# Performance work log

Hardware: AMD Instinct MI355X
Metric: run time of the kernel (lower is better)

The kernel has to match this reference:

```python
import jax, jax.numpy as jnp
import numpy as np

B, D, H = 32768, 256, 256
LEAKY = 0.2  # tf.nn.leaky_relu default alpha


def setup_inputs() -> dict:
    key = jax.random.key(0)
    ks = jax.random.split(key, 12)
    s = 0.05  # weight scale (original inits comm net to zeros; random keeps grads nonzero)
    return {
        "x": jax.random.normal(ks[0], (B, D), jnp.float32),
        "visible_states_indices": jax.random.randint(ks[1], (B, 1), 0, B, jnp.int32),
        "real_step": jnp.ones((1,), jnp.bool_),
        "h": jax.random.normal(ks[2], (B, H), jnp.float32),
        "c": jax.random.normal(ks[3], (B, H), jnp.float32),
        "W1": s * jax.random.normal(ks[4], (2 * H, 512), jnp.float32),
        "b1": jnp.zeros((512,), jnp.float32),
        "W2": s * jax.random.normal(ks[5], (512, 512), jnp.float32),
        "b2": jnp.zeros((512,), jnp.float32),
        "W3": s * jax.random.normal(ks[6], (512, H), jnp.float32),
        "b3": jnp.zeros((H,), jnp.float32),
        "Wk": s * jax.random.normal(ks[7], (D, 4 * H), jnp.float32),
        "Wr": s * jax.random.normal(ks[8], (H, 4 * H), jnp.float32),
        "bl": jnp.zeros((4 * H,), jnp.float32),
    }


def reference(x, visible_states_indices, real_step, h, c,
              W1, b1, W2, b2, W3, b3, Wk, Wr, bl):
    vid = jnp.squeeze(visible_states_indices, axis=1)          # [B]
    rs = jnp.reshape(real_step, ())                            # scalar bool

    # gather neighbor comm states with a pad row for idx == -1
    padded = jnp.pad(h, ((1, 0), (0, 0)))                      # [B+1, H]
    gathered = jnp.take(padded, vid + 1, axis=0)               # [B, H]

    cs = jnp.concatenate([h, gathered], axis=-1)               # [B, 2H]
    for W, b in ((W1, b1), (W2, b2), (W3, b3)):
        cs = jax.nn.leaky_relu(cs @ W + b, negative_slope=LEAKY)

    # conditional scatter-combine back into the h state
    final_h = jnp.where((vid >= 0)[:, None], h + cs, h)        # [B, H]

    # wrapped LSTM cell (keras LSTMCell gate ordering i, f, g, o)
    z = x @ Wk + final_h @ Wr + bl                             # [B, 4H]
    i, f, g, o = jnp.split(z, 4, axis=-1)
    c_new = jax.nn.sigmoid(f) * c + jax.nn.sigmoid(i) * jnp.tanh(g)
    h_new = jax.nn.sigmoid(o) * jnp.tanh(c_new)
    outputs = h_new

    # only commit new states on real steps
    h_out = jnp.where(rs, h_new, final_h)
    c_out = jnp.where(rs, c_new, c)
    return outputs, h_out, c_out
```

## Files before the change

### kernel.cpp

```cpp
#include <hip/hip_runtime.h>
#include <stdint.h>

#define LEAKY 0.2f
#define NB 32768
#define HD 256

typedef __attribute__((ext_vector_type(8))) short short8;
typedef __attribute__((ext_vector_type(8))) unsigned short ushort8;
typedef __attribute__((ext_vector_type(4))) float f4;

static __device__ __forceinline__ float bf2f(unsigned short u) {
  union { unsigned int i; float f; } v; v.i = ((unsigned int)u) << 16; return v.f;
}
static __device__ __forceinline__ unsigned short f2bf(float f) {
  union { float f; unsigned int i; } v; v.f = f;
  return (unsigned short)((v.i + 0x7fffu + ((v.i >> 16) & 1u)) >> 16);
}
static __device__ __forceinline__ ushort8 pack8(f4 a, f4 b) {
  ushort8 o;
  o[0] = f2bf(a[0]); o[1] = f2bf(a[1]); o[2] = f2bf(a[2]); o[3] = f2bf(a[3]);
  o[4] = f2bf(b[0]); o[5] = f2bf(b[1]); o[6] = f2bf(b[2]); o[7] = f2bf(b[3]);
  return o;
}
static __device__ __forceinline__ float sigm(float x) { return 1.f / (1.f + __expf(-x)); }
static __device__ __forceinline__ float tanha(float x) {
  float e = __expf(2.f * x);
  return 1.f - 2.f / (e + 1.f);
}

__device__ __forceinline__ void gload16(const void* g, void* s) {
  __builtin_amdgcn_global_load_lds(
      (const __attribute__((address_space(1))) unsigned int*)g,
      (__attribute__((address_space(3))) unsigned int*)s, 16, 0, 0);
}

__global__ void wprep(const float* __restrict__ W1, const float* __restrict__ W2,
                      const float* __restrict__ W3, const float* __restrict__ Wk,
                      const float* __restrict__ Wr,
                      unsigned short* __restrict__ W1t, unsigned short* __restrict__ W2t,
                      unsigned short* __restrict__ W3t, unsigned short* __restrict__ Wkrt) {
  int idx = blockIdx.x * 256 + threadIdx.x;
  if (idx < 262144) {
    int n = idx >> 9, k = idx & 511;
    W1t[idx] = f2bf(W1[k * 512 + n]);
  } else if (idx < 524288) {
    int j = idx - 262144;
    int n = j >> 9, k = j & 511;
    W2t[j] = f2bf(W2[k * 512 + n]);
  } else if (idx < 655360) {
    int j = idx - 524288;
    int n = j >> 9, k = j & 511;
    W3t[j] = f2bf(W3[k * 256 + n]);
  } else {
    int j = idx - 655360;
    int rbt = j >> 9, k = j & 511;
    int gate = (rbt >> 4) & 3;
    int hcol = (rbt >> 7) * 32 + ((rbt >> 6) & 1) * 16 + (rbt & 15);
    int ocol = gate * 256 + hcol;
    float v = (k < 256) ? Wk[k * 1024 + ocol] : Wr[(k - 256) * 1024 + ocol];
    Wkrt[j] = f2bf(v);
  }
}

__global__ void build_rows(const float* __restrict__ x, const float* __restrict__ h,
                           const int* __restrict__ vid,
                           unsigned short* __restrict__ catb,
                           unsigned short* __restrict__ csb) {
  int idx = blockIdx.x * 256 + threadIdx.x;
  int m = idx >> 5;
  int j = (idx & 31) << 3;
  f4 a0 = *(const f4*)(x + (size_t)m * 256 + j);
  f4 a1 = *(const f4*)(x + (size_t)m * 256 + j + 4);
  *(ushort8*)(catb + (size_t)m * 512 + j) = pack8(a0, a1);
  f4 h0 = *(const f4*)(h + (size_t)m * 256 + j);
  f4 h1 = *(const f4*)(h + (size_t)m * 256 + j + 4);
  *(ushort8*)(csb + (size_t)m * 512 + j) = pack8(h0, h1);
  int id = vid[m];
  f4 g0 = {0.f, 0.f, 0.f, 0.f}, g1 = {0.f, 0.f, 0.f, 0.f};
  if (id >= 0) {
    g0 = *(const f4*)(h + (size_t)id * 256 + j);
    g1 = *(const f4*)(h + (size_t)id * 256 + j + 4);
  }
  *(ushort8*)(csb + (size_t)m * 512 + 256 + j) = pack8(g0, g1);
}

template <int MODE>
__global__ __launch_bounds__(256, 2) void gemm_bf16(
    const unsigned short* __restrict__ A,
    const unsigned short* __restrict__ Bt,
    const float* __restrict__ bias,
    int nTn, int K,
    unsigned short* __restrict__ outb, int ldo, int col_off,
    float* __restrict__ outf,
    const float* __restrict__ hst,
    const int* __restrict__ vid,
    const float* __restrict__ cin,
    const unsigned char* __restrict__ rsp) {
  __shared__ unsigned short sA[128 * 64];
  __shared__ unsigned short sB[128 * 64];

  const int t = threadIdx.x;
  const int tm = blockIdx.x / nTn;
  const int tn = blockIdx.x - tm * nTn;
  const int wid = t >> 6, lane = t & 63;
  const int wr = wid >> 1, wc = wid & 1;
  const int lrow = lane & 15, lkhi = lane >> 4;

  const unsigned short* Asrc = A + (size_t)tm * 128 * K;
  const unsigned short* Bsrc = Bt + (size_t)tn * 128 * K;
  const int rsub = t >> 3, slot = t & 7;

  f4 acc[4][4];
#pragma unroll
  for (int i = 0; i < 4; ++i)
#pragma unroll
    for (int j = 0; j < 4; ++j) acc[i][j] = {0.f, 0.f, 0.f, 0.f};

  for (int k0 = 0; k0 < K; k0 += 64) {
#pragma unroll
    for (int iss = 0; iss < 4; ++iss) {
      int r = iss * 32 + rsub;
      int gs = slot ^ (r & 7);
      gload16(Asrc + (size_t)r * K + k0 + gs * 8, (char*)sA + r * 128 + slot * 16);
      gload16(Bsrc + (size_t)r * K + k0 + gs * 8, (char*)sB + r * 128 + slot * 16);
    }
    __syncthreads();
#pragma unroll
    for (int kk = 0; kk < 2; ++kk) {
      short8 af[4], bfr[4];
#pragma unroll
      for (int mi = 0; mi < 4; ++mi) {
        int row = wr * 64 + mi * 16 + lrow;
        int s = (kk * 4 + lkhi) ^ (row & 7);
        af[mi] = *(const short8*)&sA[row * 64 + s * 8];
      }
#pragma unroll
      for (int ni = 0; ni < 4; ++ni) {
        int rn = wc * 64 + ni * 16 + lrow;
        int s = (kk * 4 + lkhi) ^ (rn & 7);
        bfr[ni] = *(const short8*)&sB[rn * 64 + s * 8];
      }
#pragma unroll
      for (int mi = 0; mi < 4; ++mi)
#pragma unroll
        for (int ni = 0; ni < 4; ++ni)
          acc[mi][ni] = __builtin_amdgcn_mfma_f32_16x16x32_bf16(af[mi], bfr[ni],
                                                                acc[mi][ni], 0, 0, 0);
    }
    __syncthreads();
  }

  const int m_base = tm * 128 + wr * 64;
  const int n_base = tn * 128 + wc * 64;
  if (MODE == 1) {
#pragma unroll
    for (int mi = 0; mi < 4; ++mi) {
#pragma unroll
      for (int r = 0; r < 4; ++r) {
        int row = m_base + mi * 16 + lkhi * 4 + r;
        int id = vid[row];
#pragma unroll
        for (int ni = 0; ni < 4; ++ni) {
          int col = n_base + ni * 16 + lrow;
          float v = acc[mi][ni][r] + bias[col];
          v = v > 0.f ? v : LEAKY * v;
          float hv = hst[(size_t)row * HD + col];
          float fh = (id >= 0) ? hv + v : hv;
          outf[(size_t)row * HD + col] = fh;
          outb[(size_t)row * ldo + col_off + col] = f2bf(fh);
        }
      }
    }
  } else if (MODE == 3) {
    const bool real = rsp[0] != 0;
    const int hcol = tn * 32 + wc * 16 + lrow;
    const float bi = bias[hcol];
    const float bff = bias[256 + hcol];
    const float bg = bias[512 + hcol];
    const float bo = bias[768 + hcol];
    float* outs = outf;
    float* houtp = outf + (size_t)NB * HD;
    float* coutp = outf + (size_t)2 * NB * HD;
#pragma unroll
    for (int mi = 0; mi < 4; ++mi) {
#pragma unroll
      for (int r = 0; r < 4; ++r) {
        int row = m_base + mi * 16 + lkhi * 4 + r;
        size_t base = (size_t)row * HD + hcol;
        float cold = cin[base];
        float i_ = sigm(acc[mi][0][r] + bi);
        float f_ = sigm(acc[mi][1][r] + bff);
        float g_ = tanha(acc[mi][2][r] + bg);
        float o_ = sigm(acc[mi][3][r] + bo);
        float cv = f_ * cold + i_ * g_;
        float hv = o_ * tanha(cv);
        outs[base] = hv;
        if (real) {
          houtp[base] = hv;
          coutp[base] = cv;
        } else {
          coutp[base] = cold;
        }
      }
    }
  } else {
#pragma unroll
    for (int ni = 0; ni < 4; ++ni) {
      int col = n_base + ni * 16 + lrow;
      float bia = bias[col];
#pragma unroll
      for (int mi = 0; mi < 4; ++mi) {
#pragma unroll
        for (int r = 0; r < 4; ++r) {
          int row = m_base + mi * 16 + lkhi * 4 + r;
          float v = acc[mi][ni][r] + bia;
          v = v > 0.f ? v : LEAKY * v;
          outb[(size_t)row * ldo + col_off + col] = f2bf(v);
        }
      }
    }
  }
}

extern "C" void kernel_launch(void* const* d_in, const int* in_sizes, int n_in,
                              void* d_out, int out_size, void* d_ws, size_t ws_size,
                              hipStream_t stream) {
  const float* x = (const float*)d_in[0];
  const int* vid = (const int*)d_in[1];
  const unsigned char* rs = (const unsigned char*)d_in[2];
  const float* h = (const float*)d_in[3];
  const float* c = (const float*)d_in[4];
  const float* W1 = (const float*)d_in[5];
  const float* b1 = (const float*)d_in[6];
  const float* W2 = (const float*)d_in[7];
  const float* b2 = (const float*)d_in[8];
  const float* W3 = (const float*)d_in[9];
  const float* b3 = (const float*)d_in[10];
  const float* Wk = (const float*)d_in[11];
  const float* Wr = (const float*)d_in[12];
  const float* bl = (const float*)d_in[13];
  float* dout = (float*)d_out;

  char* ws = (char*)d_ws;
  unsigned short* W1t = (unsigned short*)(ws);
  unsigned short* W2t = (unsigned short*)(ws + 524288);
  unsigned short* W3t = (unsigned short*)(ws + 1048576);
  unsigned short* Wkrt = (unsigned short*)(ws + 1310720);
  unsigned short* bufA = (unsigned short*)(ws + 2359296);
  unsigned short* bufB = (unsigned short*)(ws + 2359296 + 33554432);
  unsigned short* catb = (unsigned short*)(ws + 2359296 + 67108864);

  float* fhout = dout + (size_t)NB * HD;

  wprep<<<4608, 256, 0, stream>>>(W1, W2, W3, Wk, Wr, W1t, W2t, W3t, Wkrt);
  build_rows<<<NB * 32 / 256, 256, 0, stream>>>(x, h, vid, catb, bufA);

  gemm_bf16<0><<<(NB / 128) * 4, 256, 0, stream>>>(
      bufA, W1t, b1, 4, 512, bufB, 512, 0, nullptr, nullptr, nullptr, nullptr, nullptr);
  gemm_bf16<0><<<(NB / 128) * 4, 256, 0, stream>>>(
      bufB, W2t, b2, 4, 512, bufA, 512, 0, nullptr, nullptr, nullptr, nullptr, nullptr);
  gemm_bf16<1><<<(NB / 128) * 2, 256, 0, stream>>>(
      bufA, W3t, b3, 2, 512, catb, 512, 256, fhout, h, vid, nullptr, nullptr);
  gemm_bf16<3><<<(NB / 128) * 8, 256, 0, stream>>>(
      catb, Wkrt, bl, 8, 512, nullptr, 0, 0, dout, nullptr, nullptr, c, rs);
}
```

Baseline: 351.3 us.

## Tile weight transpose through LDS, remap GEMM blocks per XCD, raise occupancy

The weight-prep kernel now transposes 64x64 tiles through shared memory, so reads and bf16 writes are coalesced instead of strided. The GEMM block index is remapped so that all N-tiles of one M row-tile land on the same XCD, which should improve L2 reuse of the A tile. NTN becomes a template parameter and launch bounds rise from 2 to 4 blocks per CU. The higher occupancy target may cause register spills in the 4x4 accumulator GEMM.

After: 345.2 us. No clear change (-1.7%).

```diff
diff --git a/kernel.cpp b/kernel.cpp
--- a/kernel.cpp
+++ b/kernel.cpp
@@ -39,26 +39,52 @@
                       const float* __restrict__ Wr,
                       unsigned short* __restrict__ W1t, unsigned short* __restrict__ W2t,
                       unsigned short* __restrict__ W3t, unsigned short* __restrict__ Wkrt) {
-  int idx = blockIdx.x * 256 + threadIdx.x;
-  if (idx < 262144) {
-    int n = idx >> 9, k = idx & 511;
-    W1t[idx] = f2bf(W1[k * 512 + n]);
-  } else if (idx < 524288) {
-    int j = idx - 262144;
-    int n = j >> 9, k = j & 511;
-    W2t[j] = f2bf(W2[k * 512 + n]);
-  } else if (idx < 655360) {
-    int j = idx - 524288;
-    int n = j >> 9, k = j & 511;
-    W3t[j] = f2bf(W3[k * 256 + n]);
+  __shared__ float tile[64][65];
+  const int id = blockIdx.x, t = threadIdx.x;
+  const int tr = t >> 6, tc = t & 63;
+
+  const float* src;
+  unsigned short* dst;
+  int kbase, nbase, srcld, perm = 0;
+  if (id < 64) {
+    src = W1; dst = W1t; srcld = 512;
+    kbase = (id >> 3) * 64; nbase = (id & 7) * 64;
+  } else if (id < 128) {
+    src = W2; dst = W2t; srcld = 512;
+    kbase = ((id - 64) >> 3) * 64; nbase = ((id - 64) & 7) * 64;
+  } else if (id < 160) {
+    src = W3; dst = W3t; srcld = 256;
+    kbase = ((id - 128) >> 2) * 64; nbase = ((id - 128) & 3) * 64;
   } else {
-    int j = idx - 655360;
-    int rbt = j >> 9, k = j & 511;
-    int gate = (rbt >> 4) & 3;
-    int hcol = (rbt >> 7) * 32 + ((rbt >> 6) & 1) * 16 + (rbt & 15);
-    int ocol = gate * 256 + hcol;
-    float v = (k < 256) ? Wk[k * 1024 + ocol] : Wr[(k - 256) * 1024 + ocol];
-    Wkrt[j] = f2bf(v);
+    src = nullptr; dst = Wkrt; srcld = 1024; perm = 1;
+    kbase = ((id - 160) >> 4) * 64; nbase = ((id - 160) & 15) * 64;
+  }
+
+#pragma unroll
+  for (int p = 0; p < 16; ++p) {
+    int r = p * 4 + tr;
+    int k = kbase + r, n = nbase + tc;
+    float v;
+    if (perm) {
+      v = (k < 256) ? Wk[k * 1024 + n] : Wr[(k - 256) * 1024 + n];
+    } else {
+      v = src[k * srcld + n];
+    }
+    tile[r][tc] = v;
+  }
+  __syncthreads();
+#pragma unroll
+  for (int p = 0; p < 16; ++p) {
+    int c = p * 4 + tr;
+    int n = nbase + c;
+    int orow;
+    if (perm) {
+      int gate = n >> 8, hcol = n & 255;
+      orow = (hcol >> 5) * 128 + ((hcol >> 4) & 1) * 64 + gate * 16 + (hcol & 15);
+    } else {
+      orow = n;
+    }
+    dst[orow * 512 + kbase + tc] = f2bf(tile[tc][c]);
   }
 }
 
@@ -84,12 +110,12 @@
   *(ushort8*)(csb + (size_t)m * 512 + 256 + j) = pack8(g0, g1);
 }
 
-template <int MODE>
-__global__ __launch_bounds__(256, 2) void gemm_bf16(
+template <int MODE, int NTN>
+__global__ __launch_bounds__(256, 4) void gemm_bf16(
     const unsigned short* __restrict__ A,
     const unsigned short* __restrict__ Bt,
     const float* __restrict__ bias,
-    int nTn, int K,
+    int K,
     unsigned short* __restrict__ outb, int ldo, int col_off,
     float* __restrict__ outf,
     const float* __restrict__ hst,
@@ -100,8 +126,10 @@
   __shared__ unsigned short sB[128 * 64];
 
   const int t = threadIdx.x;
-  const int tm = blockIdx.x / nTn;
-  const int tn = blockIdx.x - tm * nTn;
+  const int p = blockIdx.x;
+  const int xcd = p & 7, local = p >> 3;
+  const int tm = xcd + ((local / NTN) << 3);
+  const int tn = local % NTN;
   const int wid = t >> 6, lane = t & 63;
   const int wr = wid >> 1, wc = wid & 1;
   const int lrow = lane & 15, lkhi = lane >> 4;
@@ -252,15 +280,15 @@
 
   float* fhout = dout + (size_t)NB * HD;
 
-  wprep<<<4608, 256, 0, stream>>>(W1, W2, W3, Wk, Wr, W1t, W2t, W3t, Wkrt);
+  wprep<<<288, 256, 0, stream>>>(W1, W2, W3, Wk, Wr, W1t, W2t, W3t, Wkrt);
   build_rows<<<NB * 32 / 256, 256, 0, stream>>>(x, h, vid, catb, bufA);
 
-  gemm_bf16<0><<<(NB / 128) * 4, 256, 0, stream>>>(
-      bufA, W1t, b1, 4, 512, bufB, 512, 0, nullptr, nullptr, nullptr, nullptr, nullptr);
-  gemm_bf16<0><<<(NB / 128) * 4, 256, 0, stream>>>(
-      bufB, W2t, b2, 4, 512, bufA, 512, 0, nullptr, nullptr, nullptr, nullptr, nullptr);
-  gemm_bf16<1><<<(NB / 128) * 2, 256, 0, stream>>>(
-      bufA, W3t, b3, 2, 512, catb, 512, 256, fhout, h, vid, nullptr, nullptr);
-  gemm_bf16<3><<<(NB / 128) * 8, 256, 0, stream>>>(
-      catb, Wkrt, bl, 8, 512, nullptr, 0, 0, dout, nullptr, nullptr, c, rs);
-}
+  gemm_bf16<0, 4><<<(NB / 128) * 4, 256, 0, stream>>>(
+      bufA, W1t, b1, 512, bufB, 512, 0, nullptr, nullptr, nullptr, nullptr, nullptr);
+  gemm_bf16<0, 4><<<(NB / 128) * 4, 256, 0, stream>>>(
+      bufB, W2t, b2, 512, bufA, 512, 0, nullptr, nullptr, nullptr, nullptr, nullptr);
+  gemm_bf16<1, 2><<<(NB / 128) * 2, 256, 0, stream>>>(
+      bufA, W3t, b3, 512, catb, 512, 256, fhout, h, vid, nullptr, nullptr);
+  gemm_bf16<3, 8><<<(NB / 128) * 8, 256, 0, stream>>>(
+      catb, Wkrt, bl, 512, nullptr, 0, 0, dout, nullptr, nullptr, c, rs);
+}
```
